# Optimization experiments

Measured on AMD Instinct MI355X. Metric: run time of the kernel, lower is better.

Reference implementation:

```python
import jax, jax.numpy as jnp
import numpy as np
from jax import lax

B, T, H = 16, 4096, 512

def setup_inputs() -> dict:
    key = jax.random.key(0)
    ks = jax.random.split(key, 10)
    return {
        "query": jax.random.normal(ks[0], (B, 1, H), dtype=jnp.float32),
        "value": jax.random.normal(ks[1], (B, T, H), dtype=jnp.float32),
        "last_attn": jax.random.uniform(ks[2], (B, T), dtype=jnp.float32),
        "conv_w": jax.random.normal(ks[3], (H, 1, 3), dtype=jnp.float32) * 0.05,
        "conv_b": jax.random.normal(ks[4], (H,), dtype=jnp.float32) * 0.05,
        "Wq": jax.random.normal(ks[5], (H, H), dtype=jnp.float32) * (1.0 / np.sqrt(H)),
        "Wv": jax.random.normal(ks[6], (H, H), dtype=jnp.float32) * (1.0 / np.sqrt(H)),
        "bias": jax.random.uniform(ks[7], (H,), minval=-0.1, maxval=0.1, dtype=jnp.float32),
        "w_score": jax.random.normal(ks[8], (1, H), dtype=jnp.float32) * (1.0 / np.sqrt(H)),
        "b_score": jax.random.normal(ks[9], (1,), dtype=jnp.float32) * 0.05,
    }

def reference(query, value, last_attn, conv_w, conv_b, Wq, Wv, bias, w_score, b_score):
    # conv1d over last_attn: (B,1,T) -> (B,H,T), kernel 3, pad 1
    conv = lax.conv_general_dilated(
        last_attn[:, None, :], conv_w, window_strides=(1,), padding="SAME",
        dimension_numbers=("NCH", "OIH", "NCH"))
    conv_attn = conv.transpose(0, 2, 1) + conv_b           # (B,T,H)
    q = jnp.einsum("bqh,oh->bqo", query, Wq)               # (B,1,H), Linear w/o bias: x @ W.T
    v = jnp.einsum("bth,oh->bto", value, Wv)               # (B,T,H)
    e = jnp.tanh(q + v + conv_attn + bias)                 # (B,T,H) broadcast over q_len=1
    score = jnp.einsum("bth,h->bt", e, w_score[0]) + b_score[0]  # (B,T)
    # smoothing=True: sigmoid + L1 normalize
    s = jax.nn.sigmoid(score)
    attn = s / jnp.sum(s, axis=-1, keepdims=True)          # (B,T)
    context = jnp.einsum("bt,bth->bh", attn, value)        # (B,H)
    out = jnp.concatenate([context, query[:, 0, :]], axis=1)  # (B,2H)
    return out, attn
```

## Files before the change

kernel.cpp:

```cpp
#include <hip/hip_runtime.h>
#include <hip/hip_bf16.h>
#include <cstddef>

#define BB 16
#define TT 4096
#define HH 512

typedef _Float16 half8 __attribute__((ext_vector_type(8)));
typedef float f32x4 __attribute__((ext_vector_type(4)));

__global__ void prep_kernel(const float* __restrict__ query,
                            const float* __restrict__ conv_b,
                            const float* __restrict__ Wq,
                            const float* __restrict__ Wv,
                            const float* __restrict__ bias,
                            _Float16* __restrict__ Bpack,
                            float* __restrict__ qb,
                            float* __restrict__ ssum,
                            float* __restrict__ ctx) {
    int blk = blockIdx.x;
    int tid = threadIdx.x;
    if (blk < 32) {
        int base = blk * 8192;
        for (int i = 0; i < 32; ++i) {
            int idx = base + tid + i * 256;
            int n = idx >> 9, k = idx & 511;
            int lane = ((k >> 3) & 3) * 16 + (n & 15);
            int off = (n >> 4) * 8192 + (k >> 5) * 512 + lane * 8 + (k & 7);
            Bpack[off] = (_Float16)Wv[idx];
        }
    } else if (blk < 96) {
        int q = blk - 32;
        int b = q >> 2, oq = q & 3;
        __shared__ float qrow[HH];
        for (int i = tid; i < HH; i += 256) qrow[i] = query[b * HH + i];
        __syncthreads();
        int wave = tid >> 6, lane = tid & 63;
        float4 q1 = *(const float4*)(qrow + lane * 8);
        float4 q2 = *(const float4*)(qrow + lane * 8 + 4);
        for (int i = wave; i < 128; i += 4) {
            int o = oq * 128 + i;
            const float4* w = (const float4*)(Wq + (size_t)o * HH);
            float4 a = w[lane * 2], c = w[lane * 2 + 1];
            float acc = a.x * q1.x + a.y * q1.y + a.z * q1.z + a.w * q1.w
                      + c.x * q2.x + c.y * q2.y + c.z * q2.z + c.w * q2.w;
            #pragma unroll
            for (int off = 1; off < 64; off <<= 1) acc += __shfl_xor(acc, off, 64);
            if (lane == 0) qb[b * HH + o] = acc + bias[o] + conv_b[o];
        }
    } else {
        for (int i = tid; i < BB; i += 256) ssum[i] = 0.f;
        for (int i = tid; i < BB * HH; i += 256) ctx[i] = 0.f;
    }
}

__global__ __launch_bounds__(512, 4) void gemm_fused_kernel(
        const float* __restrict__ value,
        const float* __restrict__ last_attn,
        const float* __restrict__ conv_w,
        const float* __restrict__ w_score,
        const float* __restrict__ b_score,
        const _Float16* __restrict__ Bpack,
        const float* __restrict__ qb,
        float* __restrict__ sbuf,
        float* __restrict__ ssum,
        float* __restrict__ ctx) {
    __shared__ _Float16 As[64 * 512];
    __shared__ float sred[64][8];
    __shared__ float s_lds[64];

    int tid = threadIdx.x;
    int blk = blockIdx.x;
    int b = blk >> 6;
    int t0 = (blk & 63) << 6;

    int lane = tid & 63, ng = tid >> 6;
    int quad = lane >> 4, lm = lane & 15;
    int t = tid >> 3, g = tid & 7;

    const float* pA = value + ((size_t)(b * TT + t0 + t)) * HH + g * 16;

    f32x4 acc[4][4];
    #pragma unroll
    for (int mt = 0; mt < 4; ++mt)
        #pragma unroll
        for (int nt = 0; nt < 4; ++nt) { f32x4 z = {0.f,0.f,0.f,0.f}; acc[mt][nt] = z; }

    float4 ar[4];
    half8 breg[2][4];

    auto loadA = [&](int ck) {
        const float4* p = (const float4*)(pA + ck * 128);
        #pragma unroll
        for (int i = 0; i < 4; ++i) ar[i] = p[i];
    };
    auto writeA = [&](int ck) {
        #pragma unroll
        for (int u = 0; u < 2; ++u) {
            int c_log = ck * 16 + g * 2 + u;
            int cph = c_log ^ (t & 7);
            float4 v0 = ar[2 * u], v1 = ar[2 * u + 1];
            half8 h = { (_Float16)v0.x, (_Float16)v0.y, (_Float16)v0.z, (_Float16)v0.w,
                        (_Float16)v1.x, (_Float16)v1.y, (_Float16)v1.z, (_Float16)v1.w };
            *(half8*)(As + t * 512 + cph * 8) = h;
        }
    };
    auto loadB = [&](half8* dst, int p) {
        #pragma unroll
        for (int nt = 0; nt < 4; ++nt)
            dst[nt] = *(const half8*)(Bpack + (size_t)((ng * 4 + nt) * 16 + p) * 512 + lane * 8);
    };
    auto compute = [&](int p, const half8* bb) {
        #pragma unroll
        for (int mt = 0; mt < 4; ++mt) {
            int tr = mt * 16 + lm;
            int cph = (p * 4 + quad) ^ (tr & 7);
            half8 a = *(const half8*)(As + tr * 512 + cph * 8);
            #pragma unroll
            for (int nt = 0; nt < 4; ++nt)
                acc[mt][nt] = __builtin_amdgcn_mfma_f32_16x16x32_f16(a, bb[nt], acc[mt][nt], 0, 0, 0);
        }
    };

    loadA(0);
    loadB(breg[0], 0);
    writeA(0);
    loadA(1);
    __syncthreads();

    #pragma unroll
    for (int ck = 0; ck < 4; ++ck) {
        #pragma unroll
        for (int pp = 0; pp < 4; ++pp) {
            int p = ck * 4 + pp;
            if (p < 15) loadB(breg[(p + 1) & 1], p + 1);
            compute(p, breg[p & 1]);
        }
        if (ck < 3) {
            writeA(ck + 1);
            if (ck < 2) loadA(ck + 2);
            __syncthreads();
        }
    }

    float qvv[4], c0v[4], c1v[4], c2v[4], wvv[4];
    #pragma unroll
    for (int nt = 0; nt < 4; ++nt) {
        int o = ng * 64 + nt * 16 + lm;
        qvv[nt] = qb[b * HH + o];
        c0v[nt] = conv_w[o * 3 + 0];
        c1v[nt] = conv_w[o * 3 + 1];
        c2v[nt] = conv_w[o * 3 + 2];
        wvv[nt] = w_score[o];
    }
    float rs[4][4];
    #pragma unroll
    for (int mt = 0; mt < 4; ++mt) {
        #pragma unroll
        for (int j = 0; j < 4; ++j) {
            int tg = t0 + mt * 16 + quad * 4 + j;
            const float* la = last_attn + b * TT + tg;
            float lam = (tg > 0) ? la[-1] : 0.f;
            float la0 = la[0];
            float lap = (tg < TT - 1) ? la[1] : 0.f;
            float r = 0.f;
            #pragma unroll
            for (int nt = 0; nt < 4; ++nt) {
                float act = acc[mt][nt][j] + qvv[nt]
                          + c0v[nt] * lam + c1v[nt] * la0 + c2v[nt] * lap;
                act = fminf(15.f, fmaxf(-15.f, act));
                float e2 = __expf(2.f * act);
                r += ((e2 - 1.f) / (e2 + 1.f)) * wvv[nt];
            }
            rs[mt][j] = r;
        }
    }
    #pragma unroll
    for (int mt = 0; mt < 4; ++mt)
        #pragma unroll
        for (int j = 0; j < 4; ++j) {
            #pragma unroll
            for (int off = 1; off < 16; off <<= 1)
                rs[mt][j] += __shfl_xor(rs[mt][j], off, 64);
            if (lm == 0) sred[mt * 16 + quad * 4 + j][ng] = rs[mt][j];
        }
    __syncthreads();

    if (tid < 64) {
        float sc = b_score[0];
        #pragma unroll
        for (int k = 0; k < 8; ++k) sc += sred[tid][k];
        float s = 1.f / (1.f + __expf(-sc));
        s_lds[tid] = s;
        sbuf[b * TT + t0 + tid] = s;
        float tot = s;
        #pragma unroll
        for (int off = 1; off < 64; off <<= 1) tot += __shfl_xor(tot, off, 64);
        if (tid == 0) atomicAdd(&ssum[b], tot);
    }
    __syncthreads();

    int h = tid;
    int jh = h & 7, clh = h >> 3;
    float a = 0.f;
    #pragma unroll 8
    for (int t2 = 0; t2 < 64; ++t2) {
        int cph = clh ^ (t2 & 7);
        a += s_lds[t2] * (float)As[t2 * 512 + cph * 8 + jh];
    }
    atomicAdd(&ctx[b * HH + h], a);
}

__global__ void finalize_kernel(const float* __restrict__ query,
                                const float* __restrict__ ctx,
                                const float* __restrict__ sbuf,
                                const float* __restrict__ ssum,
                                float* __restrict__ out) {
    int idx = blockIdx.x * 256 + threadIdx.x;
    if (idx < BB * 2 * HH) {
        int b = idx >> 10, c = idx & 1023;
        float v;
        if (c < HH) v = ctx[b * HH + c] / ssum[b];
        else        v = query[b * HH + (c - HH)];
        out[idx] = v;
    } else {
        int j = idx - BB * 2 * HH;
        int b = j >> 12, t = j & 4095;
        out[idx] = sbuf[b * TT + t] / ssum[b];
    }
}

extern "C" void kernel_launch(void* const* d_in, const int* in_sizes, int n_in,
                              void* d_out, int out_size, void* d_ws, size_t ws_size,
                              hipStream_t stream) {
    const float* query     = (const float*)d_in[0];
    const float* value     = (const float*)d_in[1];
    const float* last_attn = (const float*)d_in[2];
    const float* conv_w    = (const float*)d_in[3];
    const float* conv_b    = (const float*)d_in[4];
    const float* Wq        = (const float*)d_in[5];
    const float* Wv        = (const float*)d_in[6];
    const float* bias      = (const float*)d_in[7];
    const float* w_score   = (const float*)d_in[8];
    const float* b_score   = (const float*)d_in[9];

    char* ws = (char*)d_ws;
    _Float16* Bpack = (_Float16*)ws;
    float* qb     = (float*)(ws + 524288);
    float* sbuf   = (float*)(ws + 557056);
    float* ssum   = (float*)(ws + 819200);
    float* ctx    = (float*)(ws + 819264);
    float* out    = (float*)d_out;

    prep_kernel<<<97, 256, 0, stream>>>(query, conv_b, Wq, Wv, bias, Bpack, qb, ssum, ctx);
    gemm_fused_kernel<<<1024, 512, 0, stream>>>(value, last_attn, conv_w, w_score,
                                                b_score, Bpack, qb, sbuf, ssum, ctx);
    finalize_kernel<<<320, 256, 0, stream>>>(query, ctx, sbuf, ssum, out);
}
```

Measured before the change: 295.8 us.

## Shrink GEMM tile to 32 rows, split N into two passes, vectorize Wv packing

The fused GEMM kernel now gives each block 32 time steps instead of 64. It runs 256 threads instead of 512 and launches twice as many blocks. Each block loads its whole 32x512 value tile into LDS up front, then computes the N=512 output in two halves of 256 columns, running the tanh/score epilogue after each half. This halves LDS use per block, allowing more resident blocks and removing the staged A pipeline with its repeated barriers. The trade-off is that the B weights are read from global memory twice per block and the per-block sync/atomic overhead is doubled. The prep kernel also packs Wv with vectorized float4 loads and half8 stores across 128 blocks, replacing the scalar scatter.

```diff
diff --git a/kernel.cpp b/kernel.cpp
--- a/kernel.cpp
+++ b/kernel.cpp
@@ -20,17 +20,19 @@
                             float* __restrict__ ctx) {
     int blk = blockIdx.x;
     int tid = threadIdx.x;
-    if (blk < 32) {
-        int base = blk * 8192;
-        for (int i = 0; i < 32; ++i) {
-            int idx = base + tid + i * 256;
-            int n = idx >> 9, k = idx & 511;
-            int lane = ((k >> 3) & 3) * 16 + (n & 15);
-            int off = (n >> 4) * 8192 + (k >> 5) * 512 + lane * 8 + (k & 7);
-            Bpack[off] = (_Float16)Wv[idx];
-        }
-    } else if (blk < 96) {
-        int q = blk - 32;
+    if (blk < 128) {
+        int TN = blk >> 2, kq = blk & 3;
+        int kb = kq * 4 + (tid >> 6);
+        int lane = tid & 63;
+        int n = TN * 16 + (lane & 15);
+        int k = kb * 32 + ((lane >> 4) << 3);
+        const float4* src = (const float4*)(Wv + (size_t)n * HH + k);
+        float4 v0 = src[0], v1 = src[1];
+        half8 h = { (_Float16)v0.x, (_Float16)v0.y, (_Float16)v0.z, (_Float16)v0.w,
+                    (_Float16)v1.x, (_Float16)v1.y, (_Float16)v1.z, (_Float16)v1.w };
+        *(half8*)(Bpack + (size_t)TN * 8192 + kb * 512 + lane * 8) = h;
+    } else if (blk < 192) {
+        int q = blk - 128;
         int b = q >> 2, oq = q & 3;
         __shared__ float qrow[HH];
         for (int i = tid; i < HH; i += 256) qrow[i] = query[b * HH + i];
@@ -54,7 +56,7 @@
     }
 }
 
-__global__ __launch_bounds__(512, 4) void gemm_fused_kernel(
+__global__ __launch_bounds__(256, 4) void gemm_fused_kernel(
         const float* __restrict__ value,
         const float* __restrict__ last_attn,
         const float* __restrict__ conv_w,
@@ -65,150 +67,150 @@
         float* __restrict__ sbuf,
         float* __restrict__ ssum,
         float* __restrict__ ctx) {
-    __shared__ _Float16 As[64 * 512];
-    __shared__ float sred[64][8];
-    __shared__ float s_lds[64];
+    __shared__ _Float16 As[32 * 512];
+    __shared__ float sred[32][4];
+    __shared__ float s_lds[32];
 
     int tid = threadIdx.x;
     int blk = blockIdx.x;
-    int b = blk >> 6;
-    int t0 = (blk & 63) << 6;
+    int b = blk >> 7;
+    int t0 = (blk & 127) << 5;
 
     int lane = tid & 63, ng = tid >> 6;
     int quad = lane >> 4, lm = lane & 15;
-    int t = tid >> 3, g = tid & 7;
-
-    const float* pA = value + ((size_t)(b * TT + t0 + t)) * HH + g * 16;
-
-    f32x4 acc[4][4];
-    #pragma unroll
-    for (int mt = 0; mt < 4; ++mt)
+
+    int st = tid & 31, sg = tid >> 5;
+    const float4* pA = (const float4*)(value + ((size_t)(b * TT + t0 + st)) * HH + sg * 64);
+    #pragma unroll
+    for (int u = 0; u < 8; ++u) {
+        float4 v0 = pA[2 * u], v1 = pA[2 * u + 1];
+        int cph = (sg * 8 + u) ^ (st & 7);
+        half8 h = { (_Float16)v0.x, (_Float16)v0.y, (_Float16)v0.z, (_Float16)v0.w,
+                    (_Float16)v1.x, (_Float16)v1.y, (_Float16)v1.z, (_Float16)v1.w };
+        *(half8*)(As + st * 512 + cph * 8) = h;
+    }
+
+    f32x4 acc[2][4];
+    #pragma unroll
+    for (int mt = 0; mt < 2; ++mt)
         #pragma unroll
         for (int nt = 0; nt < 4; ++nt) { f32x4 z = {0.f,0.f,0.f,0.f}; acc[mt][nt] = z; }
 
-    float4 ar[4];
     half8 breg[2][4];
-
-    auto loadA = [&](int ck) {
-        const float4* p = (const float4*)(pA + ck * 128);
-        #pragma unroll
-        for (int i = 0; i < 4; ++i) ar[i] = p[i];
+    float rs[2][4];
+    #pragma unroll
+    for (int mt = 0; mt < 2; ++mt)
+        #pragma unroll
+        for (int j = 0; j < 4; ++j) rs[mt][j] = 0.f;
+
+    const _Float16* Bbase = Bpack + lane * 8;
+
+    auto loadB = [&](half8* dst, int p, int kb) {
+        #pragma unroll
+        for (int nt = 0; nt < 4; ++nt)
+            dst[nt] = *(const half8*)(Bbase + (size_t)(((p * 16 + ng * 4 + nt) * 16 + kb) * 512));
     };
-    auto writeA = [&](int ck) {
-        #pragma unroll
-        for (int u = 0; u < 2; ++u) {
-            int c_log = ck * 16 + g * 2 + u;
-            int cph = c_log ^ (t & 7);
-            float4 v0 = ar[2 * u], v1 = ar[2 * u + 1];
-            half8 h = { (_Float16)v0.x, (_Float16)v0.y, (_Float16)v0.z, (_Float16)v0.w,
-                        (_Float16)v1.x, (_Float16)v1.y, (_Float16)v1.z, (_Float16)v1.w };
-            *(half8*)(As + t * 512 + cph * 8) = h;
-        }
-    };
-    auto loadB = [&](half8* dst, int p) {
-        #pragma unroll
-        for (int nt = 0; nt < 4; ++nt)
-            dst[nt] = *(const half8*)(Bpack + (size_t)((ng * 4 + nt) * 16 + p) * 512 + lane * 8);
-    };
-    auto compute = [&](int p, const half8* bb) {
-        #pragma unroll
-        for (int mt = 0; mt < 4; ++mt) {
+    auto compute = [&](int kb, const half8* bb) {
+        #pragma unroll
+        for (int mt = 0; mt < 2; ++mt) {
             int tr = mt * 16 + lm;
-            int cph = (p * 4 + quad) ^ (tr & 7);
+            int cph = (kb * 4 + quad) ^ (tr & 7);
             half8 a = *(const half8*)(As + tr * 512 + cph * 8);
             #pragma unroll
             for (int nt = 0; nt < 4; ++nt)
                 acc[mt][nt] = __builtin_amdgcn_mfma_f32_16x16x32_f16(a, bb[nt], acc[mt][nt], 0, 0, 0);
         }
     };
-
-    loadA(0);
-    loadB(breg[0], 0);
-    writeA(0);
-    loadA(1);
+    auto epi = [&](int p) {
+        float qvv[4], c0v[4], c1v[4], c2v[4], wvv[4];
+        #pragma unroll
+        for (int nt = 0; nt < 4; ++nt) {
+            int o = p * 256 + ng * 64 + nt * 16 + lm;
+            qvv[nt] = qb[b * HH + o];
+            c0v[nt] = conv_w[o * 3 + 0];
+            c1v[nt] = conv_w[o * 3 + 1];
+            c2v[nt] = conv_w[o * 3 + 2];
+            wvv[nt] = w_score[o];
+        }
+        #pragma unroll
+        for (int mt = 0; mt < 2; ++mt) {
+            #pragma unroll
+            for (int j = 0; j < 4; ++j) {
+                int tg = t0 + mt * 16 + quad * 4 + j;
+                const float* la = last_attn + b * TT + tg;
+                float lam = (tg > 0) ? la[-1] : 0.f;
+                float la0 = la[0];
+                float lap = (tg < TT - 1) ? la[1] : 0.f;
+                float r = 0.f;
+                #pragma unroll
+                for (int nt = 0; nt < 4; ++nt) {
+                    float act = acc[mt][nt][j] + qvv[nt]
+                              + c0v[nt] * lam + c1v[nt] * la0 + c2v[nt] * lap;
+                    act = fminf(15.f, fmaxf(-15.f, act));
+                    float e2 = __expf(2.f * act);
+                    r += ((e2 - 1.f) / (e2 + 1.f)) * wvv[nt];
+                }
+                rs[mt][j] += r;
+            }
+        }
+    };
+
+    loadB(breg[0], 0, 0);
     __syncthreads();
 
     #pragma unroll
-    for (int ck = 0; ck < 4; ++ck) {
-        #pragma unroll
-        for (int pp = 0; pp < 4; ++pp) {
-            int p = ck * 4 + pp;
-            if (p < 15) loadB(breg[(p + 1) & 1], p + 1);
-            compute(p, breg[p & 1]);
-        }
-        if (ck < 3) {
-            writeA(ck + 1);
-            if (ck < 2) loadA(ck + 2);
-            __syncthreads();
-        }
-    }
-
-    float qvv[4], c0v[4], c1v[4], c2v[4], wvv[4];
-    #pragma unroll
-    for (int nt = 0; nt < 4; ++nt) {
-        int o = ng * 64 + nt * 16 + lm;
-        qvv[nt] = qb[b * HH + o];
-        c0v[nt] = conv_w[o * 3 + 0];
-        c1v[nt] = conv_w[o * 3 + 1];
-        c2v[nt] = conv_w[o * 3 + 2];
-        wvv[nt] = w_score[o];
-    }
-    float rs[4][4];
-    #pragma unroll
-    for (int mt = 0; mt < 4; ++mt) {
+    for (int kb = 0; kb < 16; ++kb) {
+        if (kb < 15) loadB(breg[(kb + 1) & 1], 0, kb + 1);
+        else         loadB(breg[0], 1, 0);
+        compute(kb, breg[kb & 1]);
+    }
+    epi(0);
+    #pragma unroll
+    for (int mt = 0; mt < 2; ++mt)
+        #pragma unroll
+        for (int nt = 0; nt < 4; ++nt) { f32x4 z = {0.f,0.f,0.f,0.f}; acc[mt][nt] = z; }
+
+    #pragma unroll
+    for (int kb = 0; kb < 16; ++kb) {
+        if (kb < 15) loadB(breg[(kb + 1) & 1], 1, kb + 1);
+        compute(kb, breg[kb & 1]);
+    }
+    epi(1);
+
+    #pragma unroll
+    for (int mt = 0; mt < 2; ++mt)
         #pragma unroll
         for (int j = 0; j < 4; ++j) {
-            int tg = t0 + mt * 16 + quad * 4 + j;
-            const float* la = last_attn + b * TT + tg;
-            float lam = (tg > 0) ? la[-1] : 0.f;
-            float la0 = la[0];
-            float lap = (tg < TT - 1) ? la[1] : 0.f;
-            float r = 0.f;
-            #pragma unroll
-            for (int nt = 0; nt < 4; ++nt) {
-                float act = acc[mt][nt][j] + qvv[nt]
-                          + c0v[nt] * lam + c1v[nt] * la0 + c2v[nt] * lap;
-                act = fminf(15.f, fmaxf(-15.f, act));
-                float e2 = __expf(2.f * act);
-                r += ((e2 - 1.f) / (e2 + 1.f)) * wvv[nt];
-            }
-            rs[mt][j] = r;
-        }
-    }
-    #pragma unroll
-    for (int mt = 0; mt < 4; ++mt)
-        #pragma unroll
-        for (int j = 0; j < 4; ++j) {
-            #pragma unroll
-            for (int off = 1; off < 16; off <<= 1)
-                rs[mt][j] += __shfl_xor(rs[mt][j], off, 64);
-            if (lm == 0) sred[mt * 16 + quad * 4 + j][ng] = rs[mt][j];
+            float v = rs[mt][j];
+            #pragma unroll
+            for (int off = 1; off < 16; off <<= 1) v += __shfl_xor(v, off, 64);
+            if (lm == 0) sred[mt * 16 + quad * 4 + j][ng] = v;
         }
     __syncthreads();
-
-    if (tid < 64) {
-        float sc = b_score[0];
-        #pragma unroll
-        for (int k = 0; k < 8; ++k) sc += sred[tid][k];
+    if (tid < 32) {
+        float sc = b_score[0] + sred[tid][0] + sred[tid][1] + sred[tid][2] + sred[tid][3];
         float s = 1.f / (1.f + __expf(-sc));
         s_lds[tid] = s;
         sbuf[b * TT + t0 + tid] = s;
         float tot = s;
         #pragma unroll
-        for (int off = 1; off < 64; off <<= 1) tot += __shfl_xor(tot, off, 64);
+        for (int off = 1; off < 32; off <<= 1) tot += __shfl_xor(tot, off, 64);
         if (tid == 0) atomicAdd(&ssum[b], tot);
     }
     __syncthreads();
 
-    int h = tid;
-    int jh = h & 7, clh = h >> 3;
-    float a = 0.f;
-    #pragma unroll 8
-    for (int t2 = 0; t2 < 64; ++t2) {
-        int cph = clh ^ (t2 & 7);
-        a += s_lds[t2] * (float)As[t2 * 512 + cph * 8 + jh];
-    }
-    atomicAdd(&ctx[b * HH + h], a);
+    #pragma unroll
+    for (int hh = 0; hh < 2; ++hh) {
+        int h = tid + hh * 256;
+        int cl = h >> 3, j = h & 7;
+        float a = 0.f;
+        #pragma unroll 8
+        for (int t2 = 0; t2 < 32; ++t2) {
+            int cph = cl ^ (t2 & 7);
+            a += s_lds[t2] * (float)As[t2 * 512 + cph * 8 + j];
+        }
+        atomicAdd(&ctx[b * HH + h], a);
+    }
 }
 
 __global__ void finalize_kernel(const float* __restrict__ query,
@@ -252,8 +254,8 @@
     float* ctx    = (float*)(ws + 819264);
     float* out    = (float*)d_out;
 
-    prep_kernel<<<97, 256, 0, stream>>>(query, conv_b, Wq, Wv, bias, Bpack, qb, ssum, ctx);
-    gemm_fused_kernel<<<1024, 512, 0, stream>>>(value, last_attn, conv_w, w_score,
+    prep_kernel<<<193, 256, 0, stream>>>(query, conv_b, Wq, Wv, bias, Bpack, qb, ssum, ctx);
+    gemm_fused_kernel<<<2048, 256, 0, stream>>>(value, last_attn, conv_w, w_score,
                                                 b_score, Bpack, qb, sbuf, ssum, ctx);
     finalize_kernel<<<320, 256, 0, stream>>>(query, ctx, sbuf, ssum, out);
 }
```

Result: slower. 312.2 us (+5.6%).
